# Kernel tuning notes

Measured on AMD Instinct MI355X. Metric: run time of the kernel, lower is better.

Reference implementation:

```python
import jax, jax.numpy as jnp
import numpy as np

B, N, DIM, H, HD, COND, BS = 2, 1024, 768, 12, 64, 128, 16
S = 2 * N  # noised tokens [0:N) concatenated with clean x0 tokens [N:2N)
EPS = 1e-5
NEG = -1e30


def setup_inputs() -> dict:
    key = jax.random.key(0)
    ks = jax.random.split(key, 8)
    d = {}
    d['x'] = jax.random.normal(ks[0], (B, S, DIM), jnp.float32)
    d['c'] = jax.random.normal(ks[1], (B, COND), jnp.float32)
    # Rotary table for positions 0..N-1 (each half of the 2N sequence reuses the same positions)
    inv_freq = 1.0 / (10000.0 ** (np.arange(0, HD, 2, dtype=np.float64) / HD))
    freqs = np.arange(N, dtype=np.float64)[:, None] * inv_freq[None, :]
    emb = np.concatenate([freqs, freqs], axis=-1)  # [N, HD]
    cos = np.tile(np.cos(emb), (2, 1))[None, :, None, None, :]
    sin = np.tile(np.sin(emb), (2, 1))[None, :, None, None, :]
    d['cos'] = jnp.asarray(cos, jnp.float32)
    d['sin'] = jnp.asarray(sin, jnp.float32)
    # block-causal diffusion mask (flex_attention_mask): same (block, x0-flag) OR
    # cross-attention from noised block q>0 to strictly earlier CLEAN (x0) blocks
    idx = np.arange(S)
    fl = (idx >= N).astype(np.int64)
    blk = np.where(fl == 1, (idx - N) // BS, idx // BS)
    same = (blk[:, None] == blk[None, :]) & (fl[:, None] == fl[None, :])
    allowed = (blk[:, None] > 0) & (blk[None, :] < blk[:, None]) & (fl[None, :] == 1)
    d['mask'] = jnp.asarray(same | allowed)
    # parameters (adaLN is zero-init in the source; randomized here so the block is non-trivial)
    w = 0.02
    d['norm1_w'] = jnp.ones((DIM,), jnp.float32)
    d['qkv_w'] = jax.random.normal(ks[2], (3 * DIM, DIM), jnp.float32) * w
    d['attn_out_w'] = jax.random.normal(ks[3], (DIM, DIM), jnp.float32) * w
    d['norm2_w'] = jnp.ones((DIM,), jnp.float32)
    d['mlp_w1'] = jax.random.normal(ks[4], (4 * DIM, DIM), jnp.float32) * w
    d['mlp_b1'] = jnp.zeros((4 * DIM,), jnp.float32)
    d['mlp_w2'] = jax.random.normal(ks[5], (DIM, 4 * DIM), jnp.float32) * w
    d['mlp_b2'] = jnp.zeros((DIM,), jnp.float32)
    d['adaLN_w'] = jax.random.normal(ks[6], (6 * DIM, COND), jnp.float32) * w
    d['adaLN_b'] = jax.random.normal(ks[7], (6 * DIM,), jnp.float32) * w
    return d


def _ln(x, w):
    # F.layer_norm (no bias) followed by learned scale, as in the custom LayerNorm
    mu = x.mean(-1, keepdims=True)
    xc = x - mu
    var = (xc * xc).mean(-1, keepdims=True)
    return xc * jax.lax.rsqrt(var + EPS) * w


def reference(x, c, cos, sin, mask, norm1_w, qkv_w, attn_out_w, norm2_w,
              mlp_w1, mlp_b1, mlp_w2, mlp_b2, adaLN_w, adaLN_b):
    # adaLN modulation: [B, 6*DIM] -> six [B, 1, DIM] chunks
    mods = c @ adaLN_w.T + adaLN_b
    (shift_msa, scale_msa, gate_msa,
     shift_mlp, scale_mlp, gate_mlp) = jnp.split(mods[:, None, :], 6, axis=-1)
    x_skip = x
    h = _ln(x, norm1_w) * (1.0 + scale_msa) + shift_msa  # modulate_fused
    # qkv projection + rotary (torchscript path: qkv*cos + rotate_half(qkv)*sin)
    qkv = (h @ qkv_w.T).reshape(x.shape[0], S, 3, H, HD)
    rot = jnp.concatenate([-qkv[..., HD // 2:], qkv[..., :HD // 2]], axis=-1)
    qkv = qkv * cos + rot * sin
    q, k, v = qkv[:, :, 0], qkv[:, :, 1], qkv[:, :, 2]
    # SDPA with the block-causal diffusion mask, scale 1/sqrt(head_dim)
    scores = jnp.einsum('bqhd,bkhd->bhqk', q, k) / np.sqrt(HD).astype(np.float32)
    scores = jnp.where(mask[None, None], scores, NEG)
    p = jax.nn.softmax(scores, axis=-1)
    a = jnp.einsum('bhqk,bkhd->bqhd', p, v).reshape(x.shape[0], S, DIM)
    # bias_dropout_add_scale (inference => no dropout): gate * attn_out + residual
    x = gate_msa * (a @ attn_out_w.T) + x_skip
    h2 = _ln(x, norm2_w) * (1.0 + scale_mlp) + shift_mlp
    m = jax.nn.gelu(h2 @ mlp_w1.T + mlp_b1, approximate=True) @ mlp_w2.T + mlp_b2
    return x + gate_mlp * m
```

## Files before the change

### kernel.cpp

```cpp
#include <hip/hip_runtime.h>
#include <hip/hip_bf16.h>

#define EPS 1e-5f

typedef __attribute__((ext_vector_type(8))) short bf16x8;
typedef __attribute__((ext_vector_type(4))) short bf16x4;
typedef __attribute__((ext_vector_type(4))) float f32x4;

__device__ __forceinline__ f32x4 mfma_bf16(bf16x8 a, bf16x8 b, f32x4 c) {
    return __builtin_amdgcn_mfma_f32_16x16x32_bf16(a, b, c, 0, 0, 0);
}

__device__ __forceinline__ void async_ld16(const void* g, void* l) {
    __builtin_amdgcn_global_load_lds(
        (const __attribute__((address_space(1))) void*)g,
        (__attribute__((address_space(3))) void*)l, 16, 0, 0);
}

__device__ __forceinline__ float fast_gelu(float v) {
    float z2 = 1.5957691216057308f * (v + 0.044715f * v * v * v);
    float e = __expf(z2);
    return v * e / (e + 1.f);
}

__device__ __forceinline__ float bf2f(short s) {
    union { float f; unsigned u; } v;
    v.u = ((unsigned)(unsigned short)s) << 16;
    return v.f;
}

__global__ void k_pre(const float* __restrict__ a, __hip_bfloat16* __restrict__ oa, int na,
                      const float* __restrict__ b, __hip_bfloat16* __restrict__ ob, int nb,
                      const float* __restrict__ c, __hip_bfloat16* __restrict__ oc, int nc,
                      const float* __restrict__ d, __hip_bfloat16* __restrict__ od, int nd,
                      const float* __restrict__ cond, const float* __restrict__ alw,
                      const float* __restrict__ alb, float* __restrict__ mods) {
    if (blockIdx.x >= 27648) {
        int i = (blockIdx.x - 27648) * 256 + threadIdx.x;
        int bb = i / 4608, row = i - bb * 4608;
        const float4* cv = (const float4*)(cond + bb * 128);
        const float4* wv = (const float4*)(alw + (long)row * 128);
        float acc = 0.f;
#pragma unroll
        for (int k = 0; k < 32; ++k) {
            float4 x = cv[k], y = wv[k];
            acc += x.x * y.x + x.y * y.y + x.z * y.z + x.w * y.w;
        }
        mods[i] = acc + alb[row];
        return;
    }
    int i = blockIdx.x * 256 + threadIdx.x;
    if (i < na) { oa[i] = __float2bfloat16(a[i]); return; }
    i -= na;
    if (i < nb) { ob[i] = __float2bfloat16(b[i]); return; }
    i -= nb;
    if (i < nc) { oc[i] = __float2bfloat16(c[i]); return; }
    i -= nc;
    if (i < nd) od[i] = __float2bfloat16(d[i]);
}

__global__ void k_ln_mod(const float* __restrict__ x, const float* __restrict__ w,
                         const float* __restrict__ mods, int shiftOff, int scaleOff,
                         __hip_bfloat16* __restrict__ out) {
    int token = blockIdx.x;
    int lane = threadIdx.x;
    const float4* xr = (const float4*)(x + (long)token * 768);
    float4 v0 = xr[lane], v1 = xr[lane + 64], v2 = xr[lane + 128];
    float s  = v0.x + v0.y + v0.z + v0.w + v1.x + v1.y + v1.z + v1.w + v2.x + v2.y + v2.z + v2.w;
    float ss = v0.x*v0.x + v0.y*v0.y + v0.z*v0.z + v0.w*v0.w
             + v1.x*v1.x + v1.y*v1.y + v1.z*v1.z + v1.w*v1.w
             + v2.x*v2.x + v2.y*v2.y + v2.z*v2.z + v2.w*v2.w;
#pragma unroll
    for (int m = 32; m >= 1; m >>= 1) { s += __shfl_xor(s, m); ss += __shfl_xor(ss, m); }
    float mu = s * (1.f / 768.f);
    float var = ss * (1.f / 768.f) - mu * mu;
    float rs = rsqrtf(var + EPS);
    int b = token >> 11;
    const float* sh = mods + b * 4608 + shiftOff;
    const float* sc = mods + b * 4608 + scaleOff;
    __hip_bfloat16* o = out + (long)token * 768;
    float4 vv[3] = {v0, v1, v2};
#pragma unroll
    for (int kk = 0; kk < 3; ++kk) {
        int cbase = (lane + 64 * kk) * 4;
        const float* p = (const float*)&vv[kk];
#pragma unroll
        for (int j = 0; j < 4; ++j) {
            int col = cbase + j;
            float hv = (p[j] - mu) * rs * w[col] * (1.f + sc[col]) + sh[col];
            o[col] = __float2bfloat16(hv);
        }
    }
}

__global__ void k_red(const __hip_bfloat16* __restrict__ p, const float* __restrict__ x2,
                      const float* __restrict__ mods, const float* __restrict__ bias,
                      float* __restrict__ out) {
    long base = ((long)blockIdx.x * 256 + threadIdx.x) * 4;
    int col = (int)(base % 768);
    int row = (int)(base / 768);
    int b = row >> 11;
    short4 a0 = *(const short4*)(p + base);
    short4 a1 = *(const short4*)(p + 3145728 + base);
    float4 xr = *(const float4*)(x2 + base);
    float4 gt = *(const float4*)(mods + b * 4608 + 3840 + col);
    float4 bs = *(const float4*)(bias + col);
    float4 o;
    o.x = xr.x + gt.x * (bf2f(a0.x) + bf2f(a1.x) + bs.x);
    o.y = xr.y + gt.y * (bf2f(a0.y) + bf2f(a1.y) + bs.y);
    o.z = xr.z + gt.z * (bf2f(a0.z) + bf2f(a1.z) + bs.z);
    o.w = xr.w + gt.w * (bf2f(a0.w) + bf2f(a1.w) + bs.w);
    *(float4*)(out + base) = o;
}

__global__ __launch_bounds__(64) void k_attn(
    const __hip_bfloat16* __restrict__ q, const __hip_bfloat16* __restrict__ k,
    const __hip_bfloat16* __restrict__ vT, __hip_bfloat16* __restrict__ out) {
    __shared__ __hip_bfloat16 P[16 * 68];
    int lane = threadIdx.x;
    int l15 = lane & 15, quad = lane >> 4;
    int idx = blockIdx.x;
    int bh = idx % 24;
    int r = idx / 24;
    int fl, blk;
    if (r & 1) { fl = 1; blk = 63 - (r >> 1); }
    else       { fl = 0; blk = 63 - (r >> 1); }
    int qblk = fl * 64 + blk;

    const __hip_bfloat16* Q = q + ((long)bh * 2048 + qblk * 16) * 64;
    bf16x8 qa = *(const bf16x8*)(Q + l15 * 64 + quad * 8);
    bf16x8 qb = *(const bf16x8*)(Q + l15 * 64 + 32 + quad * 8);
    const __hip_bfloat16* K = k + (long)bh * 2048 * 64;
    const __hip_bfloat16* V = vT + (long)bh * 64 * 2048;

    const f32x4 vzero = {0.f, 0.f, 0.f, 0.f};
    f32x4 o[4]; float l[4];
#pragma unroll
    for (int rr = 0; rr < 4; ++rr) { o[rr] = vzero; l[rr] = 0.f; }

    int plen = (blk + fl) * 16;
    int pre = plen >> 4;
    int total16 = pre + (fl ? 0 : 1);
    int nIter = (total16 + 3) >> 2;

    auto stBase = [&](int t, bool act) -> int {
        return act ? ((t < pre) ? 1024 + t * 16 : blk * 16) : 0;
    };

    int st[4]; bool act[4];
    bf16x8 ka[4], kb8[4];
#pragma unroll
    for (int s = 0; s < 4; ++s) {
        act[s] = s < total16;
        st[s] = stBase(s, act[s]);
        const __hip_bfloat16* K0 = K + (long)st[s] * 64;
        ka[s]  = *(const bf16x8*)(K0 + l15 * 64 + quad * 8);
        kb8[s] = *(const bf16x8*)(K0 + l15 * 64 + 32 + quad * 8);
    }

    for (int ci = 0; ci < nIter; ++ci) {
        bf16x8 vf[2][4];
#pragma unroll
        for (int p2 = 0; p2 < 2; ++p2) {
            int kbv_lo = st[2 * p2], kbv_hi = st[2 * p2 + 1];
            int kbv = (quad < 2) ? kbv_lo : kbv_hi;
            int inner = (quad & 1) * 8;
#pragma unroll
            for (int tt = 0; tt < 4; ++tt)
                vf[p2][tt] = *(const bf16x8*)(V + (long)(tt * 16 + l15) * 2048 + kbv + inner);
        }

        f32x4 sc[4];
#pragma unroll
        for (int s = 0; s < 4; ++s)
            sc[s] = mfma_bf16(qb, kb8[s], mfma_bf16(qa, ka[s], vzero));

        int nst[4]; bool nact[4];
        bf16x8 nka[4], nkb[4];
        if (ci + 1 < nIter) {
#pragma unroll
            for (int s = 0; s < 4; ++s) {
                int t = 4 * (ci + 1) + s;
                nact[s] = t < total16;
                nst[s] = stBase(t, nact[s]);
                const __hip_bfloat16* K0 = K + (long)nst[s] * 64;
                nka[s] = *(const bf16x8*)(K0 + l15 * 64 + quad * 8);
                nkb[s] = *(const bf16x8*)(K0 + l15 * 64 + 32 + quad * 8);
            }
        }

#pragma unroll
        for (int s = 0; s < 4; ++s) {
#pragma unroll
            for (int rr = 0; rr < 4; ++rr) {
                float pv = act[s] ? __expf(sc[s][rr]) : 0.f;
                l[rr] += pv;
                P[(quad * 4 + rr) * 68 + s * 16 + l15] = __float2bfloat16(pv);
            }
        }
        asm volatile("s_waitcnt lgkmcnt(0)" ::: "memory");
        bf16x8 pa[2];
#pragma unroll
        for (int p2 = 0; p2 < 2; ++p2) {
            union { bf16x4 h[2]; bf16x8 v; } u;
            u.h[0] = *(const bf16x4*)(P + l15 * 68 + p2 * 32 + quad * 8);
            u.h[1] = *(const bf16x4*)(P + l15 * 68 + p2 * 32 + quad * 8 + 4);
            pa[p2] = u.v;
        }
        asm volatile("s_waitcnt lgkmcnt(0)" ::: "memory");
#pragma unroll
        for (int p2 = 0; p2 < 2; ++p2)
#pragma unroll
            for (int tt = 0; tt < 4; ++tt)
                o[tt] = mfma_bf16(pa[p2], vf[p2][tt], o[tt]);

        if (ci + 1 < nIter) {
#pragma unroll
            for (int s = 0; s < 4; ++s) {
                st[s] = nst[s]; act[s] = nact[s];
                ka[s] = nka[s]; kb8[s] = nkb[s];
            }
        }
    }

    int b = bh / 12, h = bh - b * 12;
    int seqbase = qblk * 16;
#pragma unroll
    for (int rr = 0; rr < 4; ++rr) {
        float lr = l[rr];
#pragma unroll
        for (int msk = 1; msk < 16; msk <<= 1) lr += __shfl_xor(lr, msk, 16);
        float inv = 1.f / lr;
        long row = b * 2048 + seqbase + quad * 4 + rr;
#pragma unroll
        for (int tt = 0; tt < 4; ++tt)
            out[row * 768 + h * 64 + tt * 16 + l15] = __float2bfloat16(o[tt][rr] * inv);
    }
}

template <int MODE, int TN>
__global__ __launch_bounds__(TN == 128 ? 256 : 128) void k_gemm(
    const __hip_bfloat16* __restrict__ A, const __hip_bfloat16* __restrict__ W,
    float* __restrict__ Cf, __hip_bfloat16* __restrict__ Cb,
    const float* __restrict__ bias, const float* __restrict__ mods, int gateOff,
    const float* __restrict__ resid, const float* __restrict__ cosb,
    const float* __restrict__ sinb, __hip_bfloat16* __restrict__ qo,
    __hip_bfloat16* __restrict__ ko, __hip_bfloat16* __restrict__ vo,
    int M, int N, int K, int lda) {
    constexpr int NW = (TN == 128) ? 4 : 2;
    constexpr int ACH = 512 / (NW * 64);
    constexpr int BCH = (TN * 4) / (NW * 64);
    constexpr int NINST = ACH + BCH;
    __shared__ __hip_bfloat16 lA[2][128 * 32];
    __shared__ __hip_bfloat16 lB[2][TN * 32];
    int t = threadIdx.x;
    int wave = t >> 6, lane = t & 63, l15 = lane & 15, quad = lane >> 4;
    int wr = (TN == 128) ? (wave >> 1) : wave;
    int wc = (TN == 128) ? (wave & 1) : 0;
    int sw8 = (quad ^ ((l15 >> 1) & 3)) * 8;
    long bm = blockIdx.x, bn = blockIdx.y;
    const __hip_bfloat16* Ab = A + bm * 128 * lda + (long)blockIdx.z * K;
    const __hip_bfloat16* Wb = W + bn * TN * lda + (long)blockIdx.z * K;

    long soffA[ACH], soffB[BCH];
#pragma unroll
    for (int cc = 0; cc < ACH; ++cc) {
        int chunk = cc * NW * 64 + t;
        int row = chunk >> 2;
        int c = (chunk & 3) ^ ((row >> 1) & 3);
        soffA[cc] = (long)row * lda + c * 8;
    }
#pragma unroll
    for (int cc = 0; cc < BCH; ++cc) {
        int chunk = cc * NW * 64 + t;
        int row = chunk >> 2;
        int c = (chunk & 3) ^ ((row >> 1) & 3);
        soffB[cc] = (long)row * lda + c * 8;
    }
    auto stage = [&](int k0, int buf) {
        char* lAc = (char*)&lA[buf][0];
        char* lBc = (char*)&lB[buf][0];
#pragma unroll
        for (int cc = 0; cc < ACH; ++cc)
            async_ld16(Ab + soffA[cc] + k0, lAc + cc * (NW * 1024) + wave * 1024);
#pragma unroll
        for (int cc = 0; cc < BCH; ++cc)
            async_ld16(Wb + soffB[cc] + k0, lBc + cc * (NW * 1024) + wave * 1024);
    };

    f32x4 acc[4][4];
#pragma unroll
    for (int i = 0; i < 4; ++i)
#pragma unroll
        for (int j = 0; j < 4; ++j) acc[i][j] = (f32x4){0.f, 0.f, 0.f, 0.f};

    int nIter = K / 32;
    stage(0, 0);
    for (int i = 0; i < nIter; ++i) {
        int cb = i & 1;
        if (i > 0) asm volatile("s_barrier" ::: "memory");
        if (i + 1 < nIter) {
            stage((i + 1) * 32, cb ^ 1);
            asm volatile("s_waitcnt vmcnt(%0)" :: "n"(NINST) : "memory");
        } else {
            asm volatile("s_waitcnt vmcnt(0)" ::: "memory");
        }
        asm volatile("s_barrier" ::: "memory");
        bf16x8 af[4], bfr[4];
#pragma unroll
        for (int ii = 0; ii < 4; ++ii)
            af[ii] = *(const bf16x8*)&lA[cb][(wr * 64 + ii * 16 + l15) * 32 + sw8];
#pragma unroll
        for (int j = 0; j < 4; ++j)
            bfr[j] = *(const bf16x8*)&lB[cb][(wc * 64 + j * 16 + l15) * 32 + sw8];
#pragma unroll
        for (int ii = 0; ii < 4; ++ii)
#pragma unroll
            for (int j = 0; j < 4; ++j)
                acc[ii][j] = mfma_bf16(af[ii], bfr[j], acc[ii][j]);
    }

    if (MODE == 4) {
        int hcol = (int)bn * 2 + wc;
        int th = hcol / 12, h = hcol % 12;
#pragma unroll
        for (int i = 0; i < 4; ++i) {
#pragma unroll
            for (int r = 0; r < 4; ++r) {
                int row = (int)bm * 128 + wr * 64 + i * 16 + quad * 4 + r;
                int s = row & 2047, b = row >> 11;
                long bh_ = b * 12 + h;
                const float* cbp = cosb + s * 64;
                const float* sbp = sinb + s * 64;
#pragma unroll
                for (int j = 0; j < 2; ++j) {
                    int dh = j * 16 + l15;
                    float a0f = acc[i][j][r], a1f = acc[i][j + 2][r];
                    float o0 = a0f * cbp[dh] - a1f * sbp[dh];
                    float o1 = a1f * cbp[dh + 32] + a0f * sbp[dh + 32];
                    if (th == 0) {
                        __hip_bfloat16* d = qo + (bh_ * 2048 + s) * 64;
                        d[dh]      = __float2bfloat16(o0 * 0.125f);
                        d[dh + 32] = __float2bfloat16(o1 * 0.125f);
                    } else if (th == 1) {
                        __hip_bfloat16* d = ko + (bh_ * 2048 + s) * 64;
                        d[dh]      = __float2bfloat16(o0);
                        d[dh + 32] = __float2bfloat16(o1);
                    } else {
                        __hip_bfloat16* d = vo + bh_ * 64 * 2048 + s;
                        d[(long)dh * 2048]        = __float2bfloat16(o0);
                        d[(long)(dh + 32) * 2048] = __float2bfloat16(o1);
                    }
                }
            }
        }
        return;
    }

#pragma unroll
    for (int i = 0; i < 4; ++i) {
#pragma unroll
        for (int j = 0; j < 4; ++j) {
#pragma unroll
            for (int r = 0; r < 4; ++r) {
                int row = (int)bm * 128 + wr * 64 + i * 16 + quad * 4 + r;
                int col = (int)bn * TN + wc * 64 + j * 16 + l15;
                float v = acc[i][j][r];
                long idx = (long)row * N + col;
                if (MODE == 1) {
                    Cf[idx] = mods[(row >> 11) * 4608 + gateOff + col] * v + resid[idx];
                } else if (MODE == 2) {
                    Cb[idx] = __float2bfloat16(fast_gelu(v + bias[col]));
                } else if (MODE == 3) {
                    Cf[idx] = resid[idx] + mods[(row >> 11) * 4608 + gateOff + col] * (v + bias[col]);
                } else {
                    Cb[(long)blockIdx.z * M * N + idx] = __float2bfloat16(v);
                }
            }
        }
    }
}

extern "C" void kernel_launch(void* const* d_in, const int* in_sizes, int n_in,
                              void* d_out, int out_size, void* d_ws, size_t ws_size,
                              hipStream_t stream) {
    const float* x    = (const float*)d_in[0];
    const float* c    = (const float*)d_in[1];
    const float* cosb = (const float*)d_in[2];
    const float* sinb = (const float*)d_in[3];
    const float* n1w  = (const float*)d_in[5];
    const float* qkvw = (const float*)d_in[6];
    const float* aow  = (const float*)d_in[7];
    const float* n2w  = (const float*)d_in[8];
    const float* w1   = (const float*)d_in[9];
    const float* b1   = (const float*)d_in[10];
    const float* w2   = (const float*)d_in[11];
    const float* b2   = (const float*)d_in[12];
    const float* alw  = (const float*)d_in[13];
    const float* alb  = (const float*)d_in[14];

    char* ws = (char*)d_ws;
    size_t off = 0;
    auto alloc = [&](size_t bytes) -> void* {
        void* p = ws + off;
        off += (bytes + 255) & ~(size_t)255;
        return p;
    };
    float*          mods = (float*)alloc(2 * 4608 * 4);
    __hip_bfloat16* hbuf = (__hip_bfloat16*)alloc((size_t)4096 * 768 * 2);
    __hip_bfloat16* qb   = (__hip_bfloat16*)alloc((size_t)24 * 2048 * 64 * 2);
    __hip_bfloat16* kb   = (__hip_bfloat16*)alloc((size_t)24 * 2048 * 64 * 2);
    __hip_bfloat16* vT   = (__hip_bfloat16*)alloc((size_t)24 * 64 * 2048 * 2);
    __hip_bfloat16* abuf = (__hip_bfloat16*)alloc((size_t)4096 * 768 * 2);
    float*          x2   = (float*)alloc((size_t)4096 * 768 * 4);
    __hip_bfloat16* h2   = (__hip_bfloat16*)alloc((size_t)4096 * 768 * 2);
    __hip_bfloat16* m1   = (__hip_bfloat16*)alloc((size_t)4096 * 3072 * 2);
    __hip_bfloat16* m2p  = (__hip_bfloat16*)alloc((size_t)2 * 4096 * 768 * 2);
    __hip_bfloat16* wq   = (__hip_bfloat16*)alloc((size_t)2304 * 768 * 2);
    __hip_bfloat16* wa   = (__hip_bfloat16*)alloc((size_t)768 * 768 * 2);
    __hip_bfloat16* w1b  = (__hip_bfloat16*)alloc((size_t)3072 * 768 * 2);
    __hip_bfloat16* w2b  = (__hip_bfloat16*)alloc((size_t)768 * 3072 * 2);

    k_pre<<<27684, 256, 0, stream>>>(qkvw, wq, 2304 * 768, aow, wa, 768 * 768,
                                     w1, w1b, 3072 * 768, w2, w2b, 768 * 3072,
                                     c, alw, alb, mods);
    k_ln_mod<<<4096, 64, 0, stream>>>(x, n1w, mods, 0, 768, hbuf);
    k_gemm<4, 128><<<dim3(32, 18), 256, 0, stream>>>(hbuf, wq, nullptr, nullptr, nullptr, nullptr, 0,
                                                     nullptr, cosb, sinb, qb, kb, vT,
                                                     4096, 2304, 768, 768);
    k_attn<<<3072, 64, 0, stream>>>(qb, kb, vT, abuf);
    k_gemm<1, 64><<<dim3(32, 12), 128, 0, stream>>>(abuf, wa, x2, nullptr, nullptr, mods, 1536,
                                                    x, nullptr, nullptr, nullptr, nullptr, nullptr,
                                                    4096, 768, 768, 768);
    k_ln_mod<<<4096, 64, 0, stream>>>(x2, n2w, mods, 2304, 3072, h2);
    k_gemm<2, 128><<<dim3(32, 24), 256, 0, stream>>>(h2, w1b, nullptr, m1, b1, nullptr, 0,
                                                     nullptr, nullptr, nullptr, nullptr, nullptr, nullptr,
                                                     4096, 3072, 768, 768);
    k_gemm<5, 128><<<dim3(32, 6, 2), 256, 0, stream>>>(m1, w2b, nullptr, m2p, nullptr, nullptr, 0,
                                                       nullptr, nullptr, nullptr, nullptr, nullptr, nullptr,
                                                       4096, 768, 1536, 3072);
    k_red<<<3072, 256, 0, stream>>>(m2p, x2, mods, b2, (float*)d_out);
}
```

Measured before the change: 314.4 us.

## Split attention KV range across slots and combine partials in a separate kernel

Attention for each query block is split into up to 8 slots of 8 key tiles each (split-K style). Each slot writes unnormalised bf16 partial outputs and row sums into scratch space reused from the MLP buffer. A new combine kernel sums the partials and normalises. The aim is to shorten the long serial key loops of late query blocks and balance work across CUs, at the cost of extra memory traffic, an extra launch, many early-exit blocks, and bf16 rounding of the partials. The unused GEMM MODE 3 branch is also removed.

```diff
diff --git a/kernel.cpp b/kernel.cpp
--- a/kernel.cpp
+++ b/kernel.cpp
@@ -115,16 +115,19 @@
 
 __global__ __launch_bounds__(64) void k_attn(
     const __hip_bfloat16* __restrict__ q, const __hip_bfloat16* __restrict__ k,
-    const __hip_bfloat16* __restrict__ vT, __hip_bfloat16* __restrict__ out) {
+    const __hip_bfloat16* __restrict__ vT, __hip_bfloat16* __restrict__ pO,
+    float* __restrict__ pL) {
     __shared__ __hip_bfloat16 P[16 * 68];
     int lane = threadIdx.x;
     int l15 = lane & 15, quad = lane >> 4;
-    int idx = blockIdx.x;
-    int bh = idx % 24;
-    int r = idx / 24;
+    int r = blockIdx.x;
+    int bh = blockIdx.y;
+    int slot = blockIdx.z;
     int fl, blk;
     if (r & 1) { fl = 1; blk = 63 - (r >> 1); }
     else       { fl = 0; blk = 63 - (r >> 1); }
+    int g = blk >> 3;
+    if (slot > g) return;
     int qblk = fl * 64 + blk;
 
     const __hip_bfloat16* Q = q + ((long)bh * 2048 + qblk * 16) * 64;
@@ -138,10 +141,11 @@
 #pragma unroll
     for (int rr = 0; rr < 4; ++rr) { o[rr] = vzero; l[rr] = 0.f; }
 
-    int plen = (blk + fl) * 16;
-    int pre = plen >> 4;
-    int total16 = pre + (fl ? 0 : 1);
-    int nIter = (total16 + 3) >> 2;
+    int pre = blk + fl;
+    int total16 = blk + 1;
+    int t0 = slot * 8;
+    int tEnd = min(total16, t0 + 8);
+    int nIter = (tEnd - t0 + 3) >> 2;
 
     auto stBase = [&](int t, bool act) -> int {
         return act ? ((t < pre) ? 1024 + t * 16 : blk * 16) : 0;
@@ -151,8 +155,9 @@
     bf16x8 ka[4], kb8[4];
 #pragma unroll
     for (int s = 0; s < 4; ++s) {
-        act[s] = s < total16;
-        st[s] = stBase(s, act[s]);
+        int t = t0 + s;
+        act[s] = t < tEnd;
+        st[s] = stBase(t, act[s]);
         const __hip_bfloat16* K0 = K + (long)st[s] * 64;
         ka[s]  = *(const bf16x8*)(K0 + l15 * 64 + quad * 8);
         kb8[s] = *(const bf16x8*)(K0 + l15 * 64 + 32 + quad * 8);
@@ -162,8 +167,7 @@
         bf16x8 vf[2][4];
 #pragma unroll
         for (int p2 = 0; p2 < 2; ++p2) {
-            int kbv_lo = st[2 * p2], kbv_hi = st[2 * p2 + 1];
-            int kbv = (quad < 2) ? kbv_lo : kbv_hi;
+            int kbv = (quad < 2) ? st[2 * p2] : st[2 * p2 + 1];
             int inner = (quad & 1) * 8;
 #pragma unroll
             for (int tt = 0; tt < 4; ++tt)
@@ -180,8 +184,8 @@
         if (ci + 1 < nIter) {
 #pragma unroll
             for (int s = 0; s < 4; ++s) {
-                int t = 4 * (ci + 1) + s;
-                nact[s] = t < total16;
+                int t = t0 + 4 * (ci + 1) + s;
+                nact[s] = t < tEnd;
                 nst[s] = stBase(t, nact[s]);
                 const __hip_bfloat16* K0 = K + (long)nst[s] * 64;
                 nka[s] = *(const bf16x8*)(K0 + l15 * 64 + quad * 8);
@@ -223,18 +227,48 @@
         }
     }
 
-    int b = bh / 12, h = bh - b * 12;
-    int seqbase = qblk * 16;
+    long slotIdx = (long)bh * 576 + fl * 288 + 4 * g * (g + 1) + (blk - 8 * g) * (g + 1) + slot;
+    __hip_bfloat16* po = pO + slotIdx * 1024;
 #pragma unroll
     for (int rr = 0; rr < 4; ++rr) {
         float lr = l[rr];
 #pragma unroll
         for (int msk = 1; msk < 16; msk <<= 1) lr += __shfl_xor(lr, msk, 16);
-        float inv = 1.f / lr;
-        long row = b * 2048 + seqbase + quad * 4 + rr;
+        int row = quad * 4 + rr;
+        if (l15 == 0) pL[slotIdx * 16 + row] = lr;
 #pragma unroll
         for (int tt = 0; tt < 4; ++tt)
-            out[row * 768 + h * 64 + tt * 16 + l15] = __float2bfloat16(o[tt][rr] * inv);
+            po[row * 64 + tt * 16 + l15] = __float2bfloat16(o[tt][rr]);
+    }
+}
+
+__global__ __launch_bounds__(64) void k_acomb(
+    const __hip_bfloat16* __restrict__ pO, const float* __restrict__ pL,
+    __hip_bfloat16* __restrict__ out) {
+    int idx = blockIdx.x;
+    int bh = idx >> 7, qblk = idx & 127;
+    int fl = qblk >> 6, blk = qblk & 63;
+    int g = blk >> 3, nsl = g + 1;
+    long base = (long)bh * 576 + fl * 288 + 4 * g * (g + 1) + (blk - 8 * g) * (g + 1);
+    int d = threadIdx.x;
+    float osum[16];
+    float lsum[16];
+#pragma unroll
+    for (int row = 0; row < 16; ++row) { osum[row] = 0.f; lsum[row] = 0.f; }
+    for (int s = 0; s < nsl; ++s) {
+        const __hip_bfloat16* po = pO + (base + s) * 1024;
+        const float* pl = pL + (base + s) * 16;
+#pragma unroll
+        for (int row = 0; row < 16; ++row) {
+            osum[row] += __bfloat162float(po[row * 64 + d]);
+            lsum[row] += pl[row];
+        }
+    }
+    int b = bh / 12, h = bh - b * 12;
+#pragma unroll
+    for (int row = 0; row < 16; ++row) {
+        long orow = (long)b * 2048 + qblk * 16 + row;
+        out[orow * 768 + h * 64 + d] = __float2bfloat16(osum[row] / lsum[row]);
     }
 }
 
@@ -371,8 +405,6 @@
                     Cf[idx] = mods[(row >> 11) * 4608 + gateOff + col] * v + resid[idx];
                 } else if (MODE == 2) {
                     Cb[idx] = __float2bfloat16(fast_gelu(v + bias[col]));
-                } else if (MODE == 3) {
-                    Cf[idx] = resid[idx] + mods[(row >> 11) * 4608 + gateOff + col] * (v + bias[col]);
                 } else {
                     Cb[(long)blockIdx.z * M * N + idx] = __float2bfloat16(v);
                 }
@@ -420,6 +452,8 @@
     __hip_bfloat16* wa   = (__hip_bfloat16*)alloc((size_t)768 * 768 * 2);
     __hip_bfloat16* w1b  = (__hip_bfloat16*)alloc((size_t)3072 * 768 * 2);
     __hip_bfloat16* w2b  = (__hip_bfloat16*)alloc((size_t)768 * 3072 * 2);
+    __hip_bfloat16* pO = m1;
+    float*          pL = (float*)((char*)m1 + (size_t)13824 * 1024 * 2);
 
     k_pre<<<27684, 256, 0, stream>>>(qkvw, wq, 2304 * 768, aow, wa, 768 * 768,
                                      w1, w1b, 3072 * 768, w2, w2b, 768 * 3072,
@@ -428,7 +462,8 @@
     k_gemm<4, 128><<<dim3(32, 18), 256, 0, stream>>>(hbuf, wq, nullptr, nullptr, nullptr, nullptr, 0,
                                                      nullptr, cosb, sinb, qb, kb, vT,
                                                      4096, 2304, 768, 768);
-    k_attn<<<3072, 64, 0, stream>>>(qb, kb, vT, abuf);
+    k_attn<<<dim3(128, 24, 8), 64, 0, stream>>>(qb, kb, vT, pO, pL);
+    k_acomb<<<3072, 64, 0, stream>>>(pO, pL, abuf);
     k_gemm<1, 64><<<dim3(32, 12), 128, 0, stream>>>(abuf, wa, x2, nullptr, nullptr, mods, 1536,
                                                     x, nullptr, nullptr, nullptr, nullptr, nullptr,
                                                     4096, 768, 768, 768);
```

After: 333.9 us. 1.06x slower.

## Compute transposed attention scores so P stays in registers for PV MFMA

Applied to the files above, without the earlier changes.

The attention kernel now computes S^T = K·Q^T, so each lane already holds the P fragment in the B-operand layout of a 16x16x16 MFMA. The LDS round-trip for P is removed, and PV runs as per-key-block 16x16x16 MFMAs against V fragments loaded as bf16x4. The row-sum reduction shrinks to two cross-quad shuffles. The output is transposed through LDS so global stores are coalesced. The unused MODE 3 GEMM epilogue is also dropped. In exchange, PV issues twice as many smaller MFMAs and the V loads are narrower.

```diff
diff --git a/kernel.cpp b/kernel.cpp
--- a/kernel.cpp
+++ b/kernel.cpp
@@ -9,6 +9,10 @@
 
 __device__ __forceinline__ f32x4 mfma_bf16(bf16x8 a, bf16x8 b, f32x4 c) {
     return __builtin_amdgcn_mfma_f32_16x16x32_bf16(a, b, c, 0, 0, 0);
+}
+
+__device__ __forceinline__ f32x4 mfma16_bf16(bf16x4 a, bf16x4 b, f32x4 c) {
+    return __builtin_amdgcn_mfma_f32_16x16x16bf16_1k(a, b, c, 0, 0, 0);
 }
 
 __device__ __forceinline__ void async_ld16(const void* g, void* l) {
@@ -116,7 +120,7 @@
 __global__ __launch_bounds__(64) void k_attn(
     const __hip_bfloat16* __restrict__ q, const __hip_bfloat16* __restrict__ k,
     const __hip_bfloat16* __restrict__ vT, __hip_bfloat16* __restrict__ out) {
-    __shared__ __hip_bfloat16 P[16 * 68];
+    __shared__ __hip_bfloat16 P2[16 * 68];
     int lane = threadIdx.x;
     int l15 = lane & 15, quad = lane >> 4;
     int idx = blockIdx.x;
@@ -134,13 +138,13 @@
     const __hip_bfloat16* V = vT + (long)bh * 64 * 2048;
 
     const f32x4 vzero = {0.f, 0.f, 0.f, 0.f};
-    f32x4 o[4]; float l[4];
-#pragma unroll
-    for (int rr = 0; rr < 4; ++rr) { o[rr] = vzero; l[rr] = 0.f; }
-
-    int plen = (blk + fl) * 16;
-    int pre = plen >> 4;
-    int total16 = pre + (fl ? 0 : 1);
+    f32x4 o[4];
+#pragma unroll
+    for (int tt = 0; tt < 4; ++tt) o[tt] = vzero;
+    float lsum = 0.f;
+
+    int pre = blk + fl;
+    int total16 = blk + 1;
     int nIter = (total16 + 3) >> 2;
 
     auto stBase = [&](int t, bool act) -> int {
@@ -159,21 +163,17 @@
     }
 
     for (int ci = 0; ci < nIter; ++ci) {
-        bf16x8 vf[2][4];
-#pragma unroll
-        for (int p2 = 0; p2 < 2; ++p2) {
-            int kbv_lo = st[2 * p2], kbv_hi = st[2 * p2 + 1];
-            int kbv = (quad < 2) ? kbv_lo : kbv_hi;
-            int inner = (quad & 1) * 8;
+        bf16x4 vf[4][4];
+#pragma unroll
+        for (int s = 0; s < 4; ++s)
 #pragma unroll
             for (int tt = 0; tt < 4; ++tt)
-                vf[p2][tt] = *(const bf16x8*)(V + (long)(tt * 16 + l15) * 2048 + kbv + inner);
-        }
-
-        f32x4 sc[4];
+                vf[s][tt] = *(const bf16x4*)(V + (long)(tt * 16 + l15) * 2048 + st[s] + quad * 4);
+
+        f32x4 scT[4];
 #pragma unroll
         for (int s = 0; s < 4; ++s)
-            sc[s] = mfma_bf16(qb, kb8[s], mfma_bf16(qa, ka[s], vzero));
+            scT[s] = mfma_bf16(kb8[s], qb, mfma_bf16(ka[s], qa, vzero));
 
         int nst[4]; bool nact[4];
         bf16x8 nka[4], nkb[4];
@@ -191,28 +191,18 @@
 
 #pragma unroll
         for (int s = 0; s < 4; ++s) {
+            union { short sh[4]; bf16x4 v; } pb;
 #pragma unroll
             for (int rr = 0; rr < 4; ++rr) {
-                float pv = act[s] ? __expf(sc[s][rr]) : 0.f;
-                l[rr] += pv;
-                P[(quad * 4 + rr) * 68 + s * 16 + l15] = __float2bfloat16(pv);
+                float pv = act[s] ? __expf(scT[s][rr]) : 0.f;
+                lsum += pv;
+                __hip_bfloat16 hb = __float2bfloat16(pv);
+                pb.sh[rr] = *(short*)&hb;
             }
-        }
-        asm volatile("s_waitcnt lgkmcnt(0)" ::: "memory");
-        bf16x8 pa[2];
-#pragma unroll
-        for (int p2 = 0; p2 < 2; ++p2) {
-            union { bf16x4 h[2]; bf16x8 v; } u;
-            u.h[0] = *(const bf16x4*)(P + l15 * 68 + p2 * 32 + quad * 8);
-            u.h[1] = *(const bf16x4*)(P + l15 * 68 + p2 * 32 + quad * 8 + 4);
-            pa[p2] = u.v;
-        }
-        asm volatile("s_waitcnt lgkmcnt(0)" ::: "memory");
-#pragma unroll
-        for (int p2 = 0; p2 < 2; ++p2)
 #pragma unroll
             for (int tt = 0; tt < 4; ++tt)
-                o[tt] = mfma_bf16(pa[p2], vf[p2][tt], o[tt]);
+                o[tt] = mfma16_bf16(vf[s][tt], pb.v, o[tt]);
+        }
 
         if (ci + 1 < nIter) {
 #pragma unroll
@@ -223,19 +213,22 @@
         }
     }
 
+    float lr = lsum;
+    lr += __shfl_xor(lr, 16);
+    lr += __shfl_xor(lr, 32);
+    float inv = 1.f / lr;
+
+#pragma unroll
+    for (int tt = 0; tt < 4; ++tt)
+#pragma unroll
+        for (int rr = 0; rr < 4; ++rr)
+            P2[l15 * 68 + tt * 16 + quad * 4 + rr] = __float2bfloat16(o[tt][rr] * inv);
+    asm volatile("s_waitcnt lgkmcnt(0)" ::: "memory");
     int b = bh / 12, h = bh - b * 12;
-    int seqbase = qblk * 16;
-#pragma unroll
-    for (int rr = 0; rr < 4; ++rr) {
-        float lr = l[rr];
-#pragma unroll
-        for (int msk = 1; msk < 16; msk <<= 1) lr += __shfl_xor(lr, msk, 16);
-        float inv = 1.f / lr;
-        long row = b * 2048 + seqbase + quad * 4 + rr;
-#pragma unroll
-        for (int tt = 0; tt < 4; ++tt)
-            out[row * 768 + h * 64 + tt * 16 + l15] = __float2bfloat16(o[tt][rr] * inv);
-    }
+    long base = (long)b * 2048 + qblk * 16;
+#pragma unroll
+    for (int qr = 0; qr < 16; ++qr)
+        out[(base + qr) * 768 + h * 64 + lane] = P2[qr * 68 + lane];
 }
 
 template <int MODE, int TN>
@@ -371,8 +364,6 @@
                     Cf[idx] = mods[(row >> 11) * 4608 + gateOff + col] * v + resid[idx];
                 } else if (MODE == 2) {
                     Cb[idx] = __float2bfloat16(fast_gelu(v + bias[col]));
-                } else if (MODE == 3) {
-                    Cf[idx] = resid[idx] + mods[(row >> 11) * 4608 + gateOff + col] * (v + bias[col]);
                 } else {
                     Cb[(long)blockIdx.z * M * N + idx] = __float2bfloat16(v);
                 }
```

Measured after the change: 338.1 us. +7.5%, slower.
